# Performance work log

Measured on AMD Instinct MI355X. Metric: run time of the kernel, lower is better.

The kernel has to match this reference:

```python
import jax, jax.numpy as jnp
import numpy as np

D_MODEL, D_FFN, N_LEVELS, N_HEADS, N_POINTS = 256, 1024, 4, 8, 4
B, LQ = 2, 8192
SHAPES = [(128, 128), (64, 64), (32, 32), (16, 16)]  # (H_l, W_l) per level
D_HEAD = D_MODEL // N_HEADS


def setup_inputs() -> dict:
    key = jax.random.key(0)
    ks = jax.random.split(key, 16)
    S = sum(h * w for h, w in SHAPES)

    def lin_w(k, fin, fout):
        s = 1.0 / np.sqrt(fin)
        return jax.random.uniform(k, (fin, fout), jnp.float32, -s, s)

    inp = {
        "tgt": jax.random.normal(ks[0], (B, LQ, D_MODEL), jnp.float32),
        "query_pos": jax.random.normal(ks[1], (B, LQ, D_MODEL), jnp.float32),
        "reference_points": jax.random.uniform(ks[2], (B, LQ, N_LEVELS, 2), jnp.float32),
        "src": jax.random.normal(ks[3], (B, S, D_MODEL), jnp.float32),
        "spatial_shapes": np.array(SHAPES, dtype=np.int64),
        "level_start_index": np.concatenate([[0], np.cumsum([h * w for h, w in SHAPES])[:-1]]).astype(np.int64),
        "W_value": lin_w(ks[4], D_MODEL, D_MODEL),
        "b_value": jnp.zeros((D_MODEL,), jnp.float32),
        "W_off": lin_w(ks[5], D_MODEL, N_HEADS * N_LEVELS * N_POINTS * 2),
        "b_off": 0.5 * jax.random.normal(ks[6], (N_HEADS * N_LEVELS * N_POINTS * 2,), jnp.float32),
        "W_attn": lin_w(ks[7], D_MODEL, N_HEADS * N_LEVELS * N_POINTS),
        "b_attn": jnp.zeros((N_HEADS * N_LEVELS * N_POINTS,), jnp.float32),
        "W_out": lin_w(ks[8], D_MODEL, D_MODEL),
        "b_out": jnp.zeros((D_MODEL,), jnp.float32),
        "ln1_g": jnp.ones((D_MODEL,), jnp.float32),
        "ln1_b": jnp.zeros((D_MODEL,), jnp.float32),
        "W1": lin_w(ks[9], D_MODEL, D_FFN),
        "b1": jnp.zeros((D_FFN,), jnp.float32),
        "W2": lin_w(ks[10], D_FFN, D_MODEL),
        "b2": jnp.zeros((D_MODEL,), jnp.float32),
        "ln3_g": jnp.ones((D_MODEL,), jnp.float32),
        "ln3_b": jnp.zeros((D_MODEL,), jnp.float32),
    }
    return inp


def _layer_norm(x, g, b, eps=1e-5):
    mu = jnp.mean(x, -1, keepdims=True)
    var = jnp.mean((x - mu) ** 2, -1, keepdims=True)
    return (x - mu) * jax.lax.rsqrt(var + eps) * g + b


def _ms_deform_attn(q, reference_points, src, shapes,
                    W_value, b_value, W_off, b_off, W_attn, b_attn, W_out, b_out):
    Bq, Lq, _ = q.shape
    value = (src @ W_value + b_value).reshape(Bq, -1, N_HEADS, D_HEAD)
    value = jnp.transpose(value, (0, 2, 1, 3))  # [B, H, S, Dh]
    off = (q @ W_off + b_off).reshape(Bq, Lq, N_HEADS, N_LEVELS, N_POINTS, 2)
    attn = jax.nn.softmax((q @ W_attn + b_attn).reshape(Bq, Lq, N_HEADS, N_LEVELS * N_POINTS), axis=-1)
    attn = attn.reshape(Bq, Lq, N_HEADS, N_LEVELS, N_POINTS)
    # offset normalizer is (W_l, H_l) per level
    normalizer = jnp.array([[w, h] for h, w in shapes], jnp.float32)
    loc = reference_points[:, :, None, :, None, :] + off / normalizer[None, None, None, :, None, :]

    out = jnp.zeros((Bq, Lq, N_HEADS, D_HEAD), jnp.float32)
    start = 0
    for l, (Hl, Wl) in enumerate(shapes):
        Nl = Hl * Wl
        v_l = value[:, :, start:start + Nl]  # [B, H, Nl, Dh]
        start += Nl
        loc_l = jnp.transpose(loc[:, :, :, l, :, :], (0, 2, 1, 3, 4))  # [B, H, Lq, P, 2]
        # grid_sample (align_corners=False, zero padding) pixel coords
        x = loc_l[..., 0] * Wl - 0.5
        y = loc_l[..., 1] * Hl - 0.5
        x0, y0 = jnp.floor(x), jnp.floor(y)
        wx, wy = x - x0, y - y0
        acc = jnp.zeros((Bq, N_HEADS, Lq, N_POINTS, D_HEAD), jnp.float32)
        for dx, dy, w in ((0, 0, (1 - wx) * (1 - wy)), (1, 0, wx * (1 - wy)),
                          (0, 1, (1 - wx) * wy), (1, 1, wx * wy)):
            xi, yi = x0 + dx, y0 + dy
            valid = (xi >= 0) & (xi < Wl) & (yi >= 0) & (yi < Hl)
            idx = (jnp.clip(yi, 0, Hl - 1) * Wl + jnp.clip(xi, 0, Wl - 1)).astype(jnp.int32)
            g = jnp.take_along_axis(v_l, idx.reshape(Bq, N_HEADS, -1, 1), axis=2)
            g = g.reshape(Bq, N_HEADS, Lq, N_POINTS, D_HEAD)
            acc = acc + jnp.where(valid[..., None], w[..., None] * g, 0.0)
        a = jnp.transpose(attn[:, :, :, l, :], (0, 2, 1, 3))  # [B, H, Lq, P]
        out = out + jnp.einsum('bhqp,bhqpd->bqhd', a, acc)
    return out.reshape(Bq, Lq, D_MODEL) @ W_out + b_out


def reference(tgt, query_pos, reference_points, src, spatial_shapes, level_start_index,
              W_value, b_value, W_off, b_off, W_attn, b_attn, W_out, b_out,
              ln1_g, ln1_b, W1, b1, W2, b2, ln3_g, ln3_b):
    shapes = [(int(h), int(w)) for h, w in np.asarray(spatial_shapes)]
    q = tgt + query_pos  # with_pos_embed
    tgt2 = _ms_deform_attn(q, reference_points, src, shapes,
                           W_value, b_value, W_off, b_off, W_attn, b_attn, W_out, b_out)
    x = _layer_norm(tgt + tgt2, ln1_g, ln1_b)  # dropout = identity (eval)
    ff = jax.nn.relu(x @ W1 + b1) @ W2 + b2
    return _layer_norm(x + ff, ln3_g, ln3_b)
```

## Files before the change

### kernel.cpp

```cpp
#include <hip/hip_runtime.h>
#include <hip/hip_bf16.h>
#include <hip/hip_fp16.h>
#include <math.h>

#define D_MODEL   256
#define D_FFN     1024
#define N_LEVELS  4
#define N_HEADS   8
#define N_POINTS  4
#define BATCH     2
#define LQ        8192
#define S_TOTAL   21760
#define M_Q       (BATCH*LQ)
#define M_V       (BATCH*S_TOTAL)
#define VT64      (M_V/64)

typedef __attribute__((ext_vector_type(8))) short bf16x8;
typedef __attribute__((ext_vector_type(4))) float floatx4;

struct alignas(8)  bh4 { __hip_bfloat16 a, b, c, d; };
struct alignas(16) bh8 { __hip_bfloat16 v[8]; };

__device__ __forceinline__ void gld_lds16(const void* g, void* l) {
    __builtin_amdgcn_global_load_lds(
        (const __attribute__((address_space(1))) void*)g,
        (__attribute__((address_space(3))) void*)l, 16, 0, 0);
}

__device__ __forceinline__ bh4 pack4(float4 a) {
    return { __float2bfloat16(a.x), __float2bfloat16(a.y),
             __float2bfloat16(a.z), __float2bfloat16(a.w) };
}

template<int K>
__device__ __forceinline__ void gemm_core64(const __hip_bfloat16* __restrict__ A,
                                            const __hip_bfloat16* __restrict__ Bt,
                                            int row0, int nb0, int lda, int ldb,
                                            short* As, short* Bs, floatx4 (&acc)[4])
{
    constexpr int NIT = K / 32;
    const int tid  = threadIdx.x;
    const int w    = tid >> 6;
    const int lane = tid & 63;
    const int quad = lane >> 4;
    const int l15  = lane & 15;
    const size_t ldaB = (size_t)lda * 2, ldbB = (size_t)ldb * 2;

    const int o = w * 1024 + lane * 16;
    const char* gA = (const char*)A + (size_t)(row0 + (o >> 6)) * ldaB + (o & 63);
    const char* gB = (const char*)Bt + (size_t)(nb0 + (o >> 6)) * ldbB + (o & 63);
    const int lofs = w * 512;

    gld_lds16(gA, As + lofs);
    gld_lds16(gB, Bs + lofs);

#pragma unroll 8
    for (int it = 0; it < NIT; ++it) {
        __syncthreads();
        const int cb = it & 1;
        if (it + 1 < NIT) {
            const size_t kb = (size_t)(it + 1) * 64;
            gld_lds16(gA + kb, As + (cb ^ 1) * 2048 + lofs);
            gld_lds16(gB + kb, Bs + (cb ^ 1) * 2048 + lofs);
        }
        const short* Ab = As + cb * 2048;
        const short* Bb = Bs + cb * 2048;
        bf16x8 af = *(const bf16x8*)&Ab[(w * 16 + l15) * 32 + quad * 8];
#pragma unroll
        for (int ni = 0; ni < 4; ni++) {
            bf16x8 bfr = *(const bf16x8*)&Bb[(ni * 16 + l15) * 32 + quad * 8];
            acc[ni] = __builtin_amdgcn_mfma_f32_16x16x32_bf16(af, bfr, acc[ni], 0, 0, 0);
        }
    }
}

template<int K, bool ADD>
__device__ __forceinline__ void gemm_core_cvt64(const float* __restrict__ Af,
                                                const float* __restrict__ A2f,
                                                const __hip_bfloat16* __restrict__ Bt,
                                                int row0, int nb0, int lda, int ldb,
                                                short* As, short* Bs, floatx4 (&acc)[4])
{
    constexpr int NIT = K / 32;
    const int tid  = threadIdx.x;
    const int w    = tid >> 6;
    const int lane = tid & 63;
    const int quad = lane >> 4;
    const int l15  = lane & 15;

    const int o = w * 1024 + lane * 16;
    const char* gB = (const char*)Bt + (size_t)(nb0 + (o >> 6)) * ((size_t)ldb * 2) + (o & 63);
    const int lofs = w * 512;

    const int r0 = tid >> 3, k0 = (tid & 7) * 4;
    const float* gA0 = Af + (size_t)(row0 + r0) * lda + k0;
    const float* gA1 = gA0 + (size_t)32 * lda;
    const float* gB0 = ADD ? (A2f + (size_t)(row0 + r0) * lda + k0) : nullptr;
    const float* gB1 = ADD ? (gB0 + (size_t)32 * lda) : nullptr;
    const int aofs0 = r0 * 32 + k0, aofs1 = aofs0 + 1024;

    float4 f0, f1;
    auto loadA = [&](int kt) {
        f0 = *(const float4*)(gA0 + kt);
        f1 = *(const float4*)(gA1 + kt);
        if (ADD) {
            float4 a = *(const float4*)(gB0 + kt);
            float4 b = *(const float4*)(gB1 + kt);
            f0.x += a.x; f0.y += a.y; f0.z += a.z; f0.w += a.w;
            f1.x += b.x; f1.y += b.y; f1.z += b.z; f1.w += b.w;
        }
    };
    auto writeA = [&](short* buf) {
        *(bh4*)&buf[aofs0] = pack4(f0);
        *(bh4*)&buf[aofs1] = pack4(f1);
    };

    loadA(0);
    gld_lds16(gB, Bs + lofs);
    writeA(As);

#pragma unroll 8
    for (int it = 0; it < NIT; ++it) {
        __syncthreads();
        const int cb = it & 1;
        const bool more = (it + 1 < NIT);
        if (more) {
            loadA((it + 1) * 32);
            gld_lds16(gB + (size_t)(it + 1) * 64, Bs + (cb ^ 1) * 2048 + lofs);
        }
        const short* Ab = As + cb * 2048;
        const short* Bb = Bs + cb * 2048;
        bf16x8 af = *(const bf16x8*)&Ab[(w * 16 + l15) * 32 + quad * 8];
#pragma unroll
        for (int ni = 0; ni < 4; ni++) {
            bf16x8 bfr = *(const bf16x8*)&Bb[(ni * 16 + l15) * 32 + quad * 8];
            acc[ni] = __builtin_amdgcn_mfma_f32_16x16x32_bf16(af, bfr, acc[ni], 0, 0, 0);
        }
        if (more) writeA(As + (cb ^ 1) * 2048);
    }
}

template<int K, int EPI, int COLS>
__global__ __launch_bounds__(256)
void mfma_gemm64(const __hip_bfloat16* __restrict__ A,
                 const __hip_bfloat16* __restrict__ Bt,
                 const float* __restrict__ bias,
                 float* __restrict__ outf, __hip_bfloat16* __restrict__ outb,
                 int lda, int ldb, int ldOut)
{
    __shared__ alignas(16) short As[2 * 2048];
    __shared__ alignas(16) short Bs[2 * 2048];

    constexpr int BPG = 8 * COLS;
    const int g  = blockIdx.x / BPG;
    const int wq = blockIdx.x % BPG;
    const int row0 = (g * 8 + (wq & 7)) * 64;
    const int nb0  = (wq >> 3) * 64;

    const int tid = threadIdx.x, w = tid >> 6, lane = tid & 63;
    const int quad = lane >> 4, l15 = lane & 15;

    floatx4 acc[4];
#pragma unroll
    for (int ni = 0; ni < 4; ni++) acc[ni] = (floatx4){0.f, 0.f, 0.f, 0.f};

    gemm_core64<K>(A, Bt, row0, nb0, lda, ldb, As, Bs, acc);

    float bias_c[4];
#pragma unroll
    for (int ni = 0; ni < 4; ni++) bias_c[ni] = bias ? bias[nb0 + ni * 16 + l15] : 0.f;

#pragma unroll
    for (int r = 0; r < 4; r++) {
        int row = row0 + w * 16 + quad * 4 + r;
        size_t rb = (size_t)row * ldOut + nb0;
#pragma unroll
        for (int ni = 0; ni < 4; ni++) {
            float v = acc[ni][r] + bias_c[ni];
            if (EPI == 2)      outb[rb + ni * 16 + l15] = __float2bfloat16(fmaxf(v, 0.f));
            else if (EPI == 1) outb[rb + ni * 16 + l15] = __float2bfloat16(v);
            else               outf[rb + ni * 16 + l15] = v;
        }
    }
}

__global__ __launch_bounds__(256)
void mfma_gemm_vq(const float* __restrict__ src,
                  const __hip_bfloat16* __restrict__ Wvt,
                  const float* __restrict__ b_value,
                  __hip_bfloat16* __restrict__ valueb,
                  const float* __restrict__ tgt, const float* __restrict__ qpos,
                  const __hip_bfloat16* __restrict__ Woat,
                  const float* __restrict__ b_off, const float* __restrict__ b_attn,
                  float* __restrict__ offb, float* __restrict__ attnb)
{
    __shared__ alignas(16) short As[2 * 2048];
    __shared__ alignas(16) short Bs[2 * 2048];

    const int id = blockIdx.x;
    const int tid = threadIdx.x, w = tid >> 6, lane = tid & 63;
    const int quad = lane >> 4, l15 = lane & 15;

    floatx4 acc[4];
#pragma unroll
    for (int ni = 0; ni < 4; ni++) acc[ni] = (floatx4){0.f, 0.f, 0.f, 0.f};

    if (id < VT64 * 4) {
        const int g = id >> 5, wq = id & 31;
        const int row0 = (g * 8 + (wq & 7)) * 64;
        const int nb0  = (wq >> 3) * 64;
        gemm_core_cvt64<256, false>(src, nullptr, Wvt, row0, nb0, 256, 256, As, Bs, acc);
        float bias_c[4];
#pragma unroll
        for (int ni = 0; ni < 4; ni++) bias_c[ni] = b_value[nb0 + ni * 16 + l15];
#pragma unroll
        for (int r = 0; r < 4; r++) {
            int row = row0 + w * 16 + quad * 4 + r;
            size_t rb = (size_t)row * 256 + nb0;
#pragma unroll
            for (int ni = 0; ni < 4; ni++)
                valueb[rb + ni * 16 + l15] = __float2bfloat16(acc[ni][r] + bias_c[ni]);
        }
        return;
    }

    const int oid = id - VT64 * 4;
    const int g = oid / 48, wq = oid % 48;
    const int row0 = (g * 8 + (wq & 7)) * 64;
    const int c = wq >> 3;

    if (c < 4) {
        const int nb0 = c * 64;
        gemm_core_cvt64<256, true>(tgt, qpos, Woat, row0, nb0, 256, 256, As, Bs, acc);
        float bias_c[4];
#pragma unroll
        for (int ni = 0; ni < 4; ni++) bias_c[ni] = b_off[nb0 + ni * 16 + l15];
#pragma unroll
        for (int r = 0; r < 4; r++) {
            int row = row0 + w * 16 + quad * 4 + r;
            size_t rb = (size_t)row * 256 + nb0;
#pragma unroll
            for (int ni = 0; ni < 4; ni++)
                offb[rb + ni * 16 + l15] = acc[ni][r] + bias_c[ni];
        }
    } else {
        const int c0 = (c - 4) * 64;
        gemm_core_cvt64<256, true>(tgt, qpos, Woat, row0, 256 + c0, 256, 256, As, Bs, acc);
        float bias_c[4];
#pragma unroll
        for (int ni = 0; ni < 4; ni++) bias_c[ni] = b_attn[c0 + ni * 16 + l15];
#pragma unroll
        for (int r = 0; r < 4; r++) {
            int row = row0 + w * 16 + quad * 4 + r;
            size_t rb = (size_t)row * 128 + c0;
#pragma unroll
            for (int ni = 0; ni < 4; ni++) {
                float v = acc[ni][r] + bias_c[ni];
                float m = v;
#pragma unroll
                for (int msk = 1; msk <= 8; msk <<= 1) m = fmaxf(m, __shfl_xor(m, msk));
                float e = __expf(v - m);
                float ssum = e;
#pragma unroll
                for (int msk = 1; msk <= 8; msk <<= 1) ssum += __shfl_xor(ssum, msk);
                attnb[rb + ni * 16 + l15] = e / ssum;
            }
        }
    }
}

template<bool B1>
__global__ __launch_bounds__(256)
void ln_kernel(const float* __restrict__ in1f, const __hip_bfloat16* __restrict__ in1b,
               const float* __restrict__ in2,
               const float* __restrict__ resid, const float* __restrict__ bias,
               const float* __restrict__ g, const float* __restrict__ b,
               float* __restrict__ outf, __hip_bfloat16* __restrict__ outb)
{
    const int row  = blockIdx.x * 4 + (threadIdx.x >> 6);
    const int lane = threadIdx.x & 63;
    const size_t rb = (size_t)row * 256 + lane * 4;

    float4 v = *(const float4*)(resid + rb);
    if (B1) {
        bh4 a = *(const bh4*)(in1b + rb);
        v.x += __bfloat162float(a.a); v.y += __bfloat162float(a.b);
        v.z += __bfloat162float(a.c); v.w += __bfloat162float(a.d);
    } else {
        float4 a = *(const float4*)(in1f + rb);
        v.x += a.x; v.y += a.y; v.z += a.z; v.w += a.w;
    }
    if (in2) {
        float4 c = *(const float4*)(in2 + rb);
        v.x += c.x; v.y += c.y; v.z += c.z; v.w += c.w;
    }
    if (bias) {
        float4 c = *(const float4*)(bias + lane * 4);
        v.x += c.x; v.y += c.y; v.z += c.z; v.w += c.w;
    }
    float s  = v.x + v.y + v.z + v.w;
    float sq = v.x * v.x + v.y * v.y + v.z * v.z + v.w * v.w;
#pragma unroll
    for (int msk = 1; msk <= 32; msk <<= 1) {
        s += __shfl_xor(s, msk); sq += __shfl_xor(sq, msk);
    }
    float mean = s * (1.f / 256.f);
    float var  = sq * (1.f / 256.f) - mean * mean;
    float rstd = rsqrtf(var + 1e-5f);
    float4 gg = *(const float4*)(g + lane * 4);
    float4 bb = *(const float4*)(b + lane * 4);
    float4 o;
    o.x = (v.x - mean) * rstd * gg.x + bb.x;
    o.y = (v.y - mean) * rstd * gg.y + bb.y;
    o.z = (v.z - mean) * rstd * gg.z + bb.z;
    o.w = (v.w - mean) * rstd * gg.w + bb.w;
    *(float4*)(outf + rb) = o;
    if (outb)
        *(bh4*)(outb + rb) = { __float2bfloat16(o.x), __float2bfloat16(o.y),
                               __float2bfloat16(o.z), __float2bfloat16(o.w) };
}

__global__ __launch_bounds__(256)
void prep_kernel(const float* w0, const float* w1, const float* w2,
                 const float* w3, const float* w4, const float* w5,
                 __hip_bfloat16* o0, __hip_bfloat16* o1, __hip_bfloat16* o2,
                 __hip_bfloat16* o3, __hip_bfloat16* o4, __hip_bfloat16* o5)
{
    int t = blockIdx.x;
    const float* s; __hip_bfloat16* dst; int Kd, Nd, tl;
    if      (t < 64)  { s = w0; dst = o0; Kd = 256;  Nd = 256;  tl = t; }
    else if (t < 128) { s = w1; dst = o1; Kd = 256;  Nd = 256;  tl = t - 64; }
    else if (t < 160) { s = w2; dst = o2; Kd = 256;  Nd = 128;  tl = t - 128; }
    else if (t < 224) { s = w3; dst = o3; Kd = 256;  Nd = 256;  tl = t - 160; }
    else if (t < 480) { s = w4; dst = o4; Kd = 256;  Nd = 1024; tl = t - 224; }
    else              { s = w5; dst = o5; Kd = 1024; Nd = 256;  tl = t - 480; }
    int ntn = Nd >> 5;
    int kt = tl / ntn, nt = tl - kt * ntn;
    __shared__ float T[32][33];
    int tx = threadIdx.x & 31, ty = threadIdx.x >> 5;
#pragma unroll
    for (int i = 0; i < 4; i++) {
        int k = kt * 32 + ty + i * 8;
        T[tx][ty + i * 8] = s[(size_t)k * Nd + nt * 32 + tx];
    }
    __syncthreads();
#pragma unroll
    for (int i = 0; i < 4; i++) {
        int n = nt * 32 + ty + i * 8;
        dst[(size_t)n * Kd + kt * 32 + tx] = __float2bfloat16(T[ty + i * 8][tx]);
    }
}

#define QB 8
__global__ __launch_bounds__(256, 4)
void sample_kernel(const float* __restrict__ refp, const float* __restrict__ offb,
                   const float* __restrict__ attn,
                   const __hip_bfloat16* __restrict__ value,
                   __hip_bfloat16* __restrict__ tgt2)
{
    __shared__ unsigned spk[64 * 65];

    const int q0  = blockIdx.x * QB;
    const int tid = threadIdx.x;

#pragma unroll
    for (int k = 0; k < 4; k++) {
        const int it = tid + k * 256;
        const int ql = it >> 7, h = (it >> 4) & 7, lp = it & 15;
        const int l = lp >> 2, p = lp & 3;
        const int q = q0 + ql, b = q >> 13;
        const int Wl = 128 >> l;
        const int LST = (l == 0) ? 0 : (l == 1) ? 16384 : (l == 2) ? 20480 : 21504;

        const float rx = refp[((size_t)q * N_LEVELS + l) * 2 + 0];
        const float ry = refp[((size_t)q * N_LEVELS + l) * 2 + 1];
        const float ox = offb[(size_t)q * 256 + h * 32 + l * 8 + p * 2 + 0];
        const float oy = offb[(size_t)q * 256 + h * 32 + l * 8 + p * 2 + 1];
        const float a  = attn[(size_t)q * 128 + h * 16 + lp];

        const float x = rx * Wl - 0.5f + ox;
        const float y = ry * Wl - 0.5f + oy;
        const float x0f = floorf(x), y0f = floorf(y);
        const float wx = x - x0f, wy = y - y0f;
        const int ix = (int)x0f, iy = (int)y0f;
        const int base = b * S_TOTAL + LST;
        const int g = ql * 8 + h;
        const float cw[4] = {(1.f - wx) * (1.f - wy) * a, wx * (1.f - wy) * a,
                             (1.f - wx) * wy * a,         wx * wy * a};
#pragma unroll
        for (int c = 0; c < 4; c++) {
            const int xi = ix + (c & 1), yi = iy + (c >> 1);
            const bool valid = ((unsigned)xi < (unsigned)Wl) && ((unsigned)yi < (unsigned)Wl);
            const unsigned pix = valid ? (unsigned)(base + yi * Wl + xi) : (unsigned)base;
            const __half hw = __float2half(valid ? cw[c] : 0.f);
            spk[(lp * 4 + c) * 65 + g] = (pix << 16) | (unsigned)__half_as_ushort(hw);
        }
    }
    __syncthreads();

    const int ql = tid >> 5, h = (tid >> 2) & 7, d4 = tid & 3;
    const int q = q0 + ql, g = ql * 8 + h;
    const int c0 = h * 32 + d4 * 8;
    const char* vb = (const char*)value + (size_t)c0 * 2;

    float ac[8] = {0.f, 0.f, 0.f, 0.f, 0.f, 0.f, 0.f, 0.f};
#pragma unroll
    for (int ch = 0; ch < 4; ch++) {
        unsigned us[16];
#pragma unroll
        for (int j = 0; j < 16; j++) us[j] = spk[(ch * 16 + j) * 65 + g];
        uint4 rv[16];
#pragma unroll
        for (int j = 0; j < 16; j++)
            rv[j] = *(const uint4*)(vb + ((size_t)(us[j] >> 16) << 9));
#pragma unroll
        for (int j = 0; j < 16; j++) {
            float wv = __half2float(__ushort_as_half((unsigned short)(us[j] & 0xffffu)));
            ac[0] += wv * __uint_as_float(rv[j].x << 16);
            ac[1] += wv * __uint_as_float(rv[j].x & 0xffff0000u);
            ac[2] += wv * __uint_as_float(rv[j].y << 16);
            ac[3] += wv * __uint_as_float(rv[j].y & 0xffff0000u);
            ac[4] += wv * __uint_as_float(rv[j].z << 16);
            ac[5] += wv * __uint_as_float(rv[j].z & 0xffff0000u);
            ac[6] += wv * __uint_as_float(rv[j].w << 16);
            ac[7] += wv * __uint_as_float(rv[j].w & 0xffff0000u);
        }
    }
    bh8 o;
#pragma unroll
    for (int i = 0; i < 8; i++) o.v[i] = __float2bfloat16(ac[i]);
    *(bh8*)(tgt2 + (size_t)q * 256 + c0) = o;
}

extern "C" void kernel_launch(void* const* d_in, const int* in_sizes, int n_in,
                              void* d_out, int out_size, void* d_ws, size_t ws_size,
                              hipStream_t stream) {
    const float* tgt     = (const float*)d_in[0];
    const float* qpos    = (const float*)d_in[1];
    const float* refp    = (const float*)d_in[2];
    const float* src     = (const float*)d_in[3];
    const float* W_value = (const float*)d_in[6];
    const float* b_value = (const float*)d_in[7];
    const float* W_off   = (const float*)d_in[8];
    const float* b_off   = (const float*)d_in[9];
    const float* W_attn  = (const float*)d_in[10];
    const float* b_attn  = (const float*)d_in[11];
    const float* W_out   = (const float*)d_in[12];
    const float* b_out   = (const float*)d_in[13];
    const float* ln1_g   = (const float*)d_in[14];
    const float* ln1_b   = (const float*)d_in[15];
    const float* W1      = (const float*)d_in[16];
    const float* b1      = (const float*)d_in[17];
    const float* W2      = (const float*)d_in[18];
    const float* b2      = (const float*)d_in[19];
    const float* ln3_g   = (const float*)d_in[20];
    const float* ln3_b   = (const float*)d_in[21];
    float* out = (float*)d_out;

    char* p = (char*)d_ws;
    auto nxt = [&](size_t b) { char* r = p; p += (b + 255) & ~(size_t)255; return r; };
    __hip_bfloat16* Wvt    = (__hip_bfloat16*)nxt((size_t)256 * 256 * 2);
    __hip_bfloat16* Woat   = (__hip_bfloat16*)nxt((size_t)384 * 256 * 2);
    __hip_bfloat16* Woutt  = (__hip_bfloat16*)nxt((size_t)256 * 256 * 2);
    __hip_bfloat16* W1t    = (__hip_bfloat16*)nxt((size_t)1024 * 256 * 2);
    __hip_bfloat16* W2t    = (__hip_bfloat16*)nxt((size_t)256 * 1024 * 2);
    __hip_bfloat16* valueb = (__hip_bfloat16*)nxt((size_t)M_V * 256 * 2);
    float*          offb   = (float*)nxt((size_t)M_Q * 256 * 4);
    float*          attnb  = (float*)nxt((size_t)M_Q * 128 * 4);
    __hip_bfloat16* tgt2b  = (__hip_bfloat16*)nxt((size_t)M_Q * 256 * 2);
    __hip_bfloat16* t2ob   = (__hip_bfloat16*)nxt((size_t)M_Q * 256 * 2);
    float*          x      = (float*)nxt((size_t)M_Q * 256 * 4);
    __hip_bfloat16* xb     = (__hip_bfloat16*)nxt((size_t)M_Q * 256 * 2);
    __hip_bfloat16* hb     = (__hip_bfloat16*)nxt((size_t)M_Q * 1024 * 2);
    float* f2o = (float*)valueb;

    dim3 blk(256);

    prep_kernel<<<dim3(736), blk, 0, stream>>>(
        W_value, W_off, W_attn, W_out, W1, W2,
        Wvt, Woat, Woat + 256 * 256, Woutt, W1t, W2t);

    mfma_gemm_vq<<<dim3(VT64 * 4 + 256 / 8 * 48), blk, 0, stream>>>(
        src, Wvt, b_value, valueb, tgt, qpos, Woat, b_off, b_attn, offb, attnb);

    sample_kernel<<<dim3(M_Q / QB), blk, 0, stream>>>(refp, offb, attnb, valueb, tgt2b);

    mfma_gemm64<256, 1, 4><<<dim3(M_Q / 64 * 4), blk, 0, stream>>>(
        tgt2b, Woutt, b_out, nullptr, t2ob, 256, 256, 256);

    ln_kernel<true><<<dim3(M_Q / 4), blk, 0, stream>>>(
        nullptr, t2ob, nullptr, tgt, nullptr, ln1_g, ln1_b, x, xb);

    mfma_gemm64<256, 2, 16><<<dim3(M_Q / 64 * 16), blk, 0, stream>>>(
        xb, W1t, b1, nullptr, hb, 256, 256, 1024);

    mfma_gemm64<1024, 0, 4><<<dim3(M_Q / 64 * 4), blk, 0, stream>>>(
        hb, W2t, b2, f2o, nullptr, 1024, 1024, 256);

    ln_kernel<false><<<dim3(M_Q / 4), blk, 0, stream>>>(
        f2o, nullptr, nullptr, x, nullptr, ln3_g, ln3_b, out, nullptr);
}
```

Measured before the change: 296.9 us.

## Enlarge MFMA GEMM tiles from 64x64 to 128x128 with 2x2 wave layout

All GEMM kernels, including the fused value/offset/attention projection, switch from 64x64 block tiles to 128x128 tiles. Each wave now computes a 64x64 sub-tile with 4x4 MFMA accumulators, reusing A and B fragments across more MFMAs. The aim is to cut LDS and global traffic per flop. In exchange, grid sizes shrink by four, which may underfill the GPU for the smaller GEMMs, and register and LDS pressure rise.

Measured after the change: 314.3 us. +5.8%, slower.

```diff
diff --git a/kernel.cpp b/kernel.cpp
--- a/kernel.cpp
+++ b/kernel.cpp
@@ -13,7 +13,8 @@
 #define S_TOTAL   21760
 #define M_Q       (BATCH*LQ)
 #define M_V       (BATCH*S_TOTAL)
-#define VT64      (M_V/64)
+#define VT128     (M_V/128)
+#define VQ_VAL_BLOCKS 688
 
 typedef __attribute__((ext_vector_type(8))) short bf16x8;
 typedef __attribute__((ext_vector_type(4))) float floatx4;
@@ -33,10 +34,10 @@
 }
 
 template<int K>
-__device__ __forceinline__ void gemm_core64(const __hip_bfloat16* __restrict__ A,
-                                            const __hip_bfloat16* __restrict__ Bt,
-                                            int row0, int nb0, int lda, int ldb,
-                                            short* As, short* Bs, floatx4 (&acc)[4])
+__device__ __forceinline__ void gemm_core128(const __hip_bfloat16* __restrict__ A,
+                                             const __hip_bfloat16* __restrict__ Bt,
+                                             int row0, int nb0, int lda, int ldb,
+                                             short* As, short* Bs, floatx4 (&acc)[4][4])
 {
     constexpr int NIT = K / 32;
     const int tid  = threadIdx.x;
@@ -44,15 +45,22 @@
     const int lane = tid & 63;
     const int quad = lane >> 4;
     const int l15  = lane & 15;
+    const int wr   = (w >> 1) * 64;
+    const int wc   = (w & 1) * 64;
     const size_t ldaB = (size_t)lda * 2, ldbB = (size_t)ldb * 2;
 
-    const int o = w * 1024 + lane * 16;
-    const char* gA = (const char*)A + (size_t)(row0 + (o >> 6)) * ldaB + (o & 63);
-    const char* gB = (const char*)Bt + (size_t)(nb0 + (o >> 6)) * ldbB + (o & 63);
+    const int r  = tid >> 2;
+    const int cB = (tid & 3) * 16;
+    const char* gA  = (const char*)A  + (size_t)(row0 + r) * ldaB + cB;
+    const char* gA2 = gA + 64 * ldaB;
+    const char* gB  = (const char*)Bt + (size_t)(nb0 + r) * ldbB + cB;
+    const char* gB2 = gB + 64 * ldbB;
     const int lofs = w * 512;
 
-    gld_lds16(gA, As + lofs);
-    gld_lds16(gB, Bs + lofs);
+    gld_lds16(gA,  As + lofs);
+    gld_lds16(gA2, As + 2048 + lofs);
+    gld_lds16(gB,  Bs + lofs);
+    gld_lds16(gB2, Bs + 2048 + lofs);
 
 #pragma unroll 8
     for (int it = 0; it < NIT; ++it) {
@@ -60,26 +68,33 @@
         const int cb = it & 1;
         if (it + 1 < NIT) {
             const size_t kb = (size_t)(it + 1) * 64;
-            gld_lds16(gA + kb, As + (cb ^ 1) * 2048 + lofs);
-            gld_lds16(gB + kb, Bs + (cb ^ 1) * 2048 + lofs);
-        }
-        const short* Ab = As + cb * 2048;
-        const short* Bb = Bs + cb * 2048;
-        bf16x8 af = *(const bf16x8*)&Ab[(w * 16 + l15) * 32 + quad * 8];
+            gld_lds16(gA  + kb, As + (cb ^ 1) * 4096 + lofs);
+            gld_lds16(gA2 + kb, As + (cb ^ 1) * 4096 + 2048 + lofs);
+            gld_lds16(gB  + kb, Bs + (cb ^ 1) * 4096 + lofs);
+            gld_lds16(gB2 + kb, Bs + (cb ^ 1) * 4096 + 2048 + lofs);
+        }
+        const short* Ab = As + cb * 4096;
+        const short* Bb = Bs + cb * 4096;
+        bf16x8 af[4];
+#pragma unroll
+        for (int m = 0; m < 4; m++)
+            af[m] = *(const bf16x8*)&Ab[(wr + m * 16 + l15) * 32 + quad * 8];
 #pragma unroll
         for (int ni = 0; ni < 4; ni++) {
-            bf16x8 bfr = *(const bf16x8*)&Bb[(ni * 16 + l15) * 32 + quad * 8];
-            acc[ni] = __builtin_amdgcn_mfma_f32_16x16x32_bf16(af, bfr, acc[ni], 0, 0, 0);
+            bf16x8 bfr = *(const bf16x8*)&Bb[(wc + ni * 16 + l15) * 32 + quad * 8];
+#pragma unroll
+            for (int m = 0; m < 4; m++)
+                acc[m][ni] = __builtin_amdgcn_mfma_f32_16x16x32_bf16(af[m], bfr, acc[m][ni], 0, 0, 0);
         }
     }
 }
 
 template<int K, bool ADD>
-__device__ __forceinline__ void gemm_core_cvt64(const float* __restrict__ Af,
-                                                const float* __restrict__ A2f,
-                                                const __hip_bfloat16* __restrict__ Bt,
-                                                int row0, int nb0, int lda, int ldb,
-                                                short* As, short* Bs, floatx4 (&acc)[4])
+__device__ __forceinline__ void gemm_core128_cvt(const float* __restrict__ Af,
+                                                 const float* __restrict__ A2f,
+                                                 const __hip_bfloat16* __restrict__ Bt,
+                                                 int row0, int nb0, int lda, int ldb,
+                                                 short* As, short* Bs, floatx4 (&acc)[4][4])
 {
     constexpr int NIT = K / 32;
     const int tid  = threadIdx.x;
@@ -87,36 +102,42 @@
     const int lane = tid & 63;
     const int quad = lane >> 4;
     const int l15  = lane & 15;
-
-    const int o = w * 1024 + lane * 16;
-    const char* gB = (const char*)Bt + (size_t)(nb0 + (o >> 6)) * ((size_t)ldb * 2) + (o & 63);
+    const int wr   = (w >> 1) * 64;
+    const int wc   = (w & 1) * 64;
+    const size_t ldbB = (size_t)ldb * 2;
+
+    const int r  = tid >> 2;
+    const int cB = (tid & 3) * 16;
+    const char* gB  = (const char*)Bt + (size_t)(nb0 + r) * ldbB + cB;
+    const char* gB2 = gB + 64 * ldbB;
     const int lofs = w * 512;
 
     const int r0 = tid >> 3, k0 = (tid & 7) * 4;
     const float* gA0 = Af + (size_t)(row0 + r0) * lda + k0;
-    const float* gA1 = gA0 + (size_t)32 * lda;
-    const float* gB0 = ADD ? (A2f + (size_t)(row0 + r0) * lda + k0) : nullptr;
-    const float* gB1 = ADD ? (gB0 + (size_t)32 * lda) : nullptr;
-    const int aofs0 = r0 * 32 + k0, aofs1 = aofs0 + 1024;
-
-    float4 f0, f1;
+    const float* gAd = ADD ? (A2f + (size_t)(row0 + r0) * lda + k0) : nullptr;
+
+    float4 f[4];
     auto loadA = [&](int kt) {
-        f0 = *(const float4*)(gA0 + kt);
-        f1 = *(const float4*)(gA1 + kt);
+#pragma unroll
+        for (int j = 0; j < 4; j++)
+            f[j] = *(const float4*)(gA0 + (size_t)(32 * j) * lda + kt);
         if (ADD) {
-            float4 a = *(const float4*)(gB0 + kt);
-            float4 b = *(const float4*)(gB1 + kt);
-            f0.x += a.x; f0.y += a.y; f0.z += a.z; f0.w += a.w;
-            f1.x += b.x; f1.y += b.y; f1.z += b.z; f1.w += b.w;
+#pragma unroll
+            for (int j = 0; j < 4; j++) {
+                float4 a = *(const float4*)(gAd + (size_t)(32 * j) * lda + kt);
+                f[j].x += a.x; f[j].y += a.y; f[j].z += a.z; f[j].w += a.w;
+            }
         }
     };
     auto writeA = [&](short* buf) {
-        *(bh4*)&buf[aofs0] = pack4(f0);
-        *(bh4*)&buf[aofs1] = pack4(f1);
+#pragma unroll
+        for (int j = 0; j < 4; j++)
+            *(bh4*)&buf[(r0 + 32 * j) * 32 + k0] = pack4(f[j]);
     };
 
     loadA(0);
-    gld_lds16(gB, Bs + lofs);
+    gld_lds16(gB,  Bs + lofs);
+    gld_lds16(gB2, Bs + 2048 + lofs);
     writeA(As);
 
 #pragma unroll 8
@@ -126,60 +147,72 @@
         const bool more = (it + 1 < NIT);
         if (more) {
             loadA((it + 1) * 32);
-            gld_lds16(gB + (size_t)(it + 1) * 64, Bs + (cb ^ 1) * 2048 + lofs);
-        }
-        const short* Ab = As + cb * 2048;
-        const short* Bb = Bs + cb * 2048;
-        bf16x8 af = *(const bf16x8*)&Ab[(w * 16 + l15) * 32 + quad * 8];
+            gld_lds16(gB  + (size_t)(it + 1) * 64, Bs + (cb ^ 1) * 4096 + lofs);
+            gld_lds16(gB2 + (size_t)(it + 1) * 64, Bs + (cb ^ 1) * 4096 + 2048 + lofs);
+        }
+        const short* Ab = As + cb * 4096;
+        const short* Bb = Bs + cb * 4096;
+        bf16x8 af[4];
+#pragma unroll
+        for (int m = 0; m < 4; m++)
+            af[m] = *(const bf16x8*)&Ab[(wr + m * 16 + l15) * 32 + quad * 8];
 #pragma unroll
         for (int ni = 0; ni < 4; ni++) {
-            bf16x8 bfr = *(const bf16x8*)&Bb[(ni * 16 + l15) * 32 + quad * 8];
-            acc[ni] = __builtin_amdgcn_mfma_f32_16x16x32_bf16(af, bfr, acc[ni], 0, 0, 0);
-        }
-        if (more) writeA(As + (cb ^ 1) * 2048);
+            bf16x8 bfr = *(const bf16x8*)&Bb[(wc + ni * 16 + l15) * 32 + quad * 8];
+#pragma unroll
+            for (int m = 0; m < 4; m++)
+                acc[m][ni] = __builtin_amdgcn_mfma_f32_16x16x32_bf16(af[m], bfr, acc[m][ni], 0, 0, 0);
+        }
+        if (more) writeA(As + (cb ^ 1) * 4096);
     }
 }
 
 template<int K, int EPI, int COLS>
 __global__ __launch_bounds__(256)
-void mfma_gemm64(const __hip_bfloat16* __restrict__ A,
-                 const __hip_bfloat16* __restrict__ Bt,
-                 const float* __restrict__ bias,
-                 float* __restrict__ outf, __hip_bfloat16* __restrict__ outb,
-                 int lda, int ldb, int ldOut)
-{
-    __shared__ alignas(16) short As[2 * 2048];
-    __shared__ alignas(16) short Bs[2 * 2048];
+void mfma_gemm128(const __hip_bfloat16* __restrict__ A,
+                  const __hip_bfloat16* __restrict__ Bt,
+                  const float* __restrict__ bias,
+                  float* __restrict__ outf, __hip_bfloat16* __restrict__ outb,
+                  int lda, int ldb, int ldOut)
+{
+    __shared__ alignas(16) short As[2 * 4096];
+    __shared__ alignas(16) short Bs[2 * 4096];
 
     constexpr int BPG = 8 * COLS;
     const int g  = blockIdx.x / BPG;
     const int wq = blockIdx.x % BPG;
-    const int row0 = (g * 8 + (wq & 7)) * 64;
-    const int nb0  = (wq >> 3) * 64;
+    const int row0 = (g * 8 + (wq & 7)) * 128;
+    const int nb0  = (wq >> 3) * 128;
 
     const int tid = threadIdx.x, w = tid >> 6, lane = tid & 63;
     const int quad = lane >> 4, l15 = lane & 15;
-
-    floatx4 acc[4];
-#pragma unroll
-    for (int ni = 0; ni < 4; ni++) acc[ni] = (floatx4){0.f, 0.f, 0.f, 0.f};
-
-    gemm_core64<K>(A, Bt, row0, nb0, lda, ldb, As, Bs, acc);
+    const int wr = (w >> 1) * 64, wc = (w & 1) * 64;
+
+    floatx4 acc[4][4];
+#pragma unroll
+    for (int m = 0; m < 4; m++)
+#pragma unroll
+        for (int ni = 0; ni < 4; ni++) acc[m][ni] = (floatx4){0.f, 0.f, 0.f, 0.f};
+
+    gemm_core128<K>(A, Bt, row0, nb0, lda, ldb, As, Bs, acc);
 
     float bias_c[4];
 #pragma unroll
-    for (int ni = 0; ni < 4; ni++) bias_c[ni] = bias ? bias[nb0 + ni * 16 + l15] : 0.f;
-
-#pragma unroll
-    for (int r = 0; r < 4; r++) {
-        int row = row0 + w * 16 + quad * 4 + r;
-        size_t rb = (size_t)row * ldOut + nb0;
-#pragma unroll
-        for (int ni = 0; ni < 4; ni++) {
-            float v = acc[ni][r] + bias_c[ni];
-            if (EPI == 2)      outb[rb + ni * 16 + l15] = __float2bfloat16(fmaxf(v, 0.f));
-            else if (EPI == 1) outb[rb + ni * 16 + l15] = __float2bfloat16(v);
-            else               outf[rb + ni * 16 + l15] = v;
+    for (int ni = 0; ni < 4; ni++) bias_c[ni] = bias ? bias[nb0 + wc + ni * 16 + l15] : 0.f;
+
+#pragma unroll
+    for (int m = 0; m < 4; m++) {
+#pragma unroll
+        for (int rr = 0; rr < 4; rr++) {
+            int row = row0 + wr + m * 16 + quad * 4 + rr;
+            size_t rb = (size_t)row * ldOut + nb0 + wc;
+#pragma unroll
+            for (int ni = 0; ni < 4; ni++) {
+                float v = acc[m][ni][rr] + bias_c[ni];
+                if (EPI == 2)      outb[rb + ni * 16 + l15] = __float2bfloat16(fmaxf(v, 0.f));
+                else if (EPI == 1) outb[rb + ni * 16 + l15] = __float2bfloat16(v);
+                else               outf[rb + ni * 16 + l15] = v;
+            }
         }
     }
 }
@@ -194,76 +227,89 @@
                   const float* __restrict__ b_off, const float* __restrict__ b_attn,
                   float* __restrict__ offb, float* __restrict__ attnb)
 {
-    __shared__ alignas(16) short As[2 * 2048];
-    __shared__ alignas(16) short Bs[2 * 2048];
+    __shared__ alignas(16) short As[2 * 4096];
+    __shared__ alignas(16) short Bs[2 * 4096];
 
     const int id = blockIdx.x;
     const int tid = threadIdx.x, w = tid >> 6, lane = tid & 63;
     const int quad = lane >> 4, l15 = lane & 15;
-
-    floatx4 acc[4];
-#pragma unroll
-    for (int ni = 0; ni < 4; ni++) acc[ni] = (floatx4){0.f, 0.f, 0.f, 0.f};
-
-    if (id < VT64 * 4) {
-        const int g = id >> 5, wq = id & 31;
-        const int row0 = (g * 8 + (wq & 7)) * 64;
-        const int nb0  = (wq >> 3) * 64;
-        gemm_core_cvt64<256, false>(src, nullptr, Wvt, row0, nb0, 256, 256, As, Bs, acc);
+    const int wr = (w >> 1) * 64, wc = (w & 1) * 64;
+
+    floatx4 acc[4][4];
+#pragma unroll
+    for (int m = 0; m < 4; m++)
+#pragma unroll
+        for (int ni = 0; ni < 4; ni++) acc[m][ni] = (floatx4){0.f, 0.f, 0.f, 0.f};
+
+    if (id < VQ_VAL_BLOCKS) {
+        const int g = id >> 4, wq = id & 15;
+        const int rt = g * 8 + (wq & 7);
+        if (rt >= VT128) return;
+        const int row0 = rt * 128;
+        const int nb0  = (wq >> 3) * 128;
+        gemm_core128_cvt<256, false>(src, nullptr, Wvt, row0, nb0, 256, 256, As, Bs, acc);
         float bias_c[4];
 #pragma unroll
-        for (int ni = 0; ni < 4; ni++) bias_c[ni] = b_value[nb0 + ni * 16 + l15];
-#pragma unroll
-        for (int r = 0; r < 4; r++) {
-            int row = row0 + w * 16 + quad * 4 + r;
-            size_t rb = (size_t)row * 256 + nb0;
-#pragma unroll
-            for (int ni = 0; ni < 4; ni++)
-                valueb[rb + ni * 16 + l15] = __float2bfloat16(acc[ni][r] + bias_c[ni]);
+        for (int ni = 0; ni < 4; ni++) bias_c[ni] = b_value[nb0 + wc + ni * 16 + l15];
+#pragma unroll
+        for (int m = 0; m < 4; m++) {
+#pragma unroll
+            for (int rr = 0; rr < 4; rr++) {
+                int row = row0 + wr + m * 16 + quad * 4 + rr;
+                size_t rb = (size_t)row * 256 + nb0 + wc;
+#pragma unroll
+                for (int ni = 0; ni < 4; ni++)
+                    valueb[rb + ni * 16 + l15] = __float2bfloat16(acc[m][ni][rr] + bias_c[ni]);
+            }
         }
         return;
     }
 
-    const int oid = id - VT64 * 4;
-    const int g = oid / 48, wq = oid % 48;
-    const int row0 = (g * 8 + (wq & 7)) * 64;
+    const int oid = id - VQ_VAL_BLOCKS;
+    const int g = oid / 24, wq = oid % 24;
+    const int row0 = (g * 8 + (wq & 7)) * 128;
     const int c = wq >> 3;
 
-    if (c < 4) {
-        const int nb0 = c * 64;
-        gemm_core_cvt64<256, true>(tgt, qpos, Woat, row0, nb0, 256, 256, As, Bs, acc);
+    if (c < 2) {
+        const int nb0 = c * 128;
+        gemm_core128_cvt<256, true>(tgt, qpos, Woat, row0, nb0, 256, 256, As, Bs, acc);
         float bias_c[4];
 #pragma unroll
-        for (int ni = 0; ni < 4; ni++) bias_c[ni] = b_off[nb0 + ni * 16 + l15];
-#pragma unroll
-        for (int r = 0; r < 4; r++) {
-            int row = row0 + w * 16 + quad * 4 + r;
-            size_t rb = (size_t)row * 256 + nb0;
-#pragma unroll
-            for (int ni = 0; ni < 4; ni++)
-                offb[rb + ni * 16 + l15] = acc[ni][r] + bias_c[ni];
+        for (int ni = 0; ni < 4; ni++) bias_c[ni] = b_off[nb0 + wc + ni * 16 + l15];
+#pragma unroll
+        for (int m = 0; m < 4; m++) {
+#pragma unroll
+            for (int rr = 0; rr < 4; rr++) {
+                int row = row0 + wr + m * 16 + quad * 4 + rr;
+                size_t rb = (size_t)row * 256 + nb0 + wc;
+#pragma unroll
+                for (int ni = 0; ni < 4; ni++)
+                    offb[rb + ni * 16 + l15] = acc[m][ni][rr] + bias_c[ni];
+            }
         }
     } else {
-        const int c0 = (c - 4) * 64;
-        gemm_core_cvt64<256, true>(tgt, qpos, Woat, row0, 256 + c0, 256, 256, As, Bs, acc);
+        gemm_core128_cvt<256, true>(tgt, qpos, Woat, row0, 256, 256, 256, As, Bs, acc);
         float bias_c[4];
 #pragma unroll
-        for (int ni = 0; ni < 4; ni++) bias_c[ni] = b_attn[c0 + ni * 16 + l15];
-#pragma unroll
-        for (int r = 0; r < 4; r++) {
-            int row = row0 + w * 16 + quad * 4 + r;
-            size_t rb = (size_t)row * 128 + c0;
-#pragma unroll
-            for (int ni = 0; ni < 4; ni++) {
-                float v = acc[ni][r] + bias_c[ni];
-                float m = v;
-#pragma unroll
-                for (int msk = 1; msk <= 8; msk <<= 1) m = fmaxf(m, __shfl_xor(m, msk));
-                float e = __expf(v - m);
-                float ssum = e;
-#pragma unroll
-                for (int msk = 1; msk <= 8; msk <<= 1) ssum += __shfl_xor(ssum, msk);
-                attnb[rb + ni * 16 + l15] = e / ssum;
+        for (int ni = 0; ni < 4; ni++) bias_c[ni] = b_attn[wc + ni * 16 + l15];
+#pragma unroll
+        for (int m = 0; m < 4; m++) {
+#pragma unroll
+            for (int rr = 0; rr < 4; rr++) {
+                int row = row0 + wr + m * 16 + quad * 4 + rr;
+                size_t rb = (size_t)row * 128 + wc;
+#pragma unroll
+                for (int ni = 0; ni < 4; ni++) {
+                    float v = acc[m][ni][rr] + bias_c[ni];
+                    float mx = v;
+#pragma unroll
+                    for (int msk = 1; msk <= 8; msk <<= 1) mx = fmaxf(mx, __shfl_xor(mx, msk));
+                    float e = __expf(v - mx);
+                    float ssum = e;
+#pragma unroll
+                    for (int msk = 1; msk <= 8; msk <<= 1) ssum += __shfl_xor(ssum, msk);
+                    attnb[rb + ni * 16 + l15] = e / ssum;
+                }
             }
         }
     }
@@ -480,21 +526,21 @@
         W_value, W_off, W_attn, W_out, W1, W2,
         Wvt, Woat, Woat + 256 * 256, Woutt, W1t, W2t);
 
-    mfma_gemm_vq<<<dim3(VT64 * 4 + 256 / 8 * 48), blk, 0, stream>>>(
+    mfma_gemm_vq<<<dim3(VQ_VAL_BLOCKS + 16 * 24), blk, 0, stream>>>(
         src, Wvt, b_value, valueb, tgt, qpos, Woat, b_off, b_attn, offb, attnb);
 
     sample_kernel<<<dim3(M_Q / QB), blk, 0, stream>>>(refp, offb, attnb, valueb, tgt2b);
 
-    mfma_gemm64<256, 1, 4><<<dim3(M_Q / 64 * 4), blk, 0, stream>>>(
+    mfma_gemm128<256, 1, 2><<<dim3(M_Q / 128 * 2), blk, 0, stream>>>(
         tgt2b, Woutt, b_out, nullptr, t2ob, 256, 256, 256);
 
     ln_kernel<true><<<dim3(M_Q / 4), blk, 0, stream>>>(
         nullptr, t2ob, nullptr, tgt, nullptr, ln1_g, ln1_b, x, xb);
 
-    mfma_gemm64<256, 2, 16><<<dim3(M_Q / 64 * 16), blk, 0, stream>>>(
+    mfma_gemm128<256, 2, 8><<<dim3(M_Q / 128 * 8), blk, 0, stream>>>(
         xb, W1t, b1, nullptr, hb, 256, 256, 1024);
 
-    mfma_gemm64<1024, 0, 4><<<dim3(M_Q / 64 * 4), blk, 0, stream>>>(
+    mfma_gemm128<1024, 0, 2><<<dim3(M_Q / 128 * 2), blk, 0, stream>>>(
         hb, W2t, b2, f2o, nullptr, 1024, 1024, 256);
 
     ln_kernel<false><<<dim3(M_Q / 4), blk, 0, stream>>>(
```
